# Kernel tuning notes

Measured on AMD Instinct MI355X. Metric: run time of the kernel, lower is better.

## Reference

```python
import jax, jax.numpy as jnp
import numpy as np

N = 471
TOPK = 50
T = 16384
M = 128


def setup_inputs() -> dict:
    key = jax.random.key(0)
    ks = jax.random.split(key, 6)
    x = jax.random.normal(ks[0], (T, N), dtype=jnp.float32)
    q_t = jax.random.normal(ks[1], (M, N), dtype=jnp.float32)
    # parameters, initialized as in the torch module
    w = 0.0021 + 0.0005 * jax.random.normal(ks[2], (N,), dtype=jnp.float32)
    b1 = jax.random.normal(ks[3], (N,), dtype=jnp.float32)  # unused in forward math
    alpha = jnp.array([10.0], dtype=jnp.float32)
    lamda = jnp.array([0.1], dtype=jnp.float32)
    rho = jnp.array([0.001], dtype=jnp.float32)
    mu = jnp.array([0.001], dtype=jnp.float32)
    bound = 1.0 / np.sqrt(N)
    linear_w = jax.random.uniform(ks[4], (N, N), minval=-bound, maxval=bound, dtype=jnp.float32)
    linear_b = jax.random.uniform(ks[5], (N,), minval=-bound, maxval=bound, dtype=jnp.float32)
    return {"x": x, "q_t": q_t, "w": w, "b1": b1, "alpha": alpha,
            "lamda": lamda, "rho": rho, "mu": mu,
            "linear_w": linear_w, "linear_b": linear_b}


def reference(x, q_t, w, b1, alpha, lamda, rho, mu, linear_w, linear_b):
    # W2 = mean over time of Linear(x); identical every unrolled iteration -> compute once
    W2 = (x @ linear_w.T + linear_b).mean(axis=0)           # [N]
    pinvQ = jnp.linalg.pinv(q_t @ q_t.T)                    # [M,M], identical every iter

    def theta_update(z, u):
        v = u - rho * (z - w)                               # [N]
        return alpha * (pinvQ @ (q_t @ v))                  # [M]

    def z_update(z, u, theta):
        b = w + (q_t.T @ theta) / N                         # [N]
        grad_z = W2 + rho * (z - b) + u
        grad_z = grad_z + 2.0 * lamda * (jnp.sum(z) - 1.0)  # scalar * ones broadcast
        grad_z = grad_z + 2.0 * lamda * jnp.minimum(0.0, z)
        z_new = jax.nn.relu(z - mu * grad_z)
        _, idx = jax.lax.top_k(z_new, TOPK)
        mask = jnp.zeros_like(z_new).at[idx].set(1.0)
        return z_new * mask

    z = jnp.zeros(N, dtype=x.dtype)
    u = jnp.zeros(N, dtype=x.dtype)
    for _ in range(9):
        theta = theta_update(z, u)
        z = z_update(z, u, theta)
        b = w + (q_t.T @ theta) / N
        u = u + rho * (z - b)
    theta = theta_update(z, u)
    z = z_update(z, u, theta)
    return z / (jnp.sum(z) + 1e-8)
```

## Files before the change

kernel.cpp:

```cpp
#include <hip/hip_runtime.h>

#define NDIM 471
#define MD   128
#define TD   16384
#define KSEL 50
#define CGIT 4

#define WS_PART   0
#define WS_G      120832
#define WS_T1     137216
#define WS_XBAR   197888
#define WS_W2     198400
#define WS_RW     198912
#define WS_CTR    199384
#define WS_R      199424

static __device__ __forceinline__ float rdl(float v, int lane){
    return __int_as_float(__builtin_amdgcn_readlane(__float_as_int(v), lane));
}

__global__ __launch_bounds__(512) void k_gram_colsum(const float* __restrict__ qt,
                                                     const float* __restrict__ x,
                                                     const float* __restrict__ wv,
                                                     float* __restrict__ ws){
    int lane = threadIdx.x & 63, wid = threadIdx.x >> 6;
    if (blockIdx.x < 256){
        float* G = ws + WS_G;
        int gw = blockIdx.x * 8 + wid;
        int i = gw >> 4, jb = gw & 15;
        float qi[8];
#pragma unroll
        for (int s = 0; s < 8; ++s){ int idx = lane + 64*s; qi[s] = (idx < NDIM) ? qt[i*NDIM + idx] : 0.f; }
#pragma unroll
        for (int t = 0; t < 8; ++t){
            int j = jb + 16*t;
            float acc = 0.f;
#pragma unroll
            for (int s = 0; s < 8; ++s){
                int idx = lane + 64*s;
                float qj = (idx < NDIM) ? qt[j*NDIM + idx] : 0.f;
                acc = fmaf(qi[s], qj, acc);
            }
#pragma unroll
            for (int d = 1; d < 64; d <<= 1) acc += __shfl_xor(acc, d);
            if (lane == 0) G[i*MD + j] = acc;
        }
    } else {
        int cb = blockIdx.x - 256;
        int col = threadIdx.x;
        if (col < NDIM){
            const float* xp = x + (size_t)cb*64*NDIM + col;
            float acc = 0.f;
#pragma unroll 4
            for (int r = 0; r < 64; ++r) acc += xp[(size_t)r*NDIM];
            ws[WS_PART + cb*NDIM + col] = acc;
        }
        if (cb < 16){
            int m = cb*8 + wid;
            float acc = 0.f;
#pragma unroll
            for (int s = 0; s < 8; ++s){
                int idx = lane + 64*s;
                if (idx < NDIM) acc = fmaf(qt[m*NDIM + idx], wv[idx], acc);
            }
#pragma unroll
            for (int d = 1; d < 64; d <<= 1) acc += __shfl_xor(acc, d);
            if (lane == 0) ws[WS_T1 + m] = acc;
        }
    }
}

#define G_LD(n) float4 t##n = *(const float4*)(Gp + 4*(n)); \
                float Ga##n = t##n.x, Gb##n = t##n.y, Gc##n = t##n.z, Gd##n = t##n.w;
#define G_DOT(n) pa = fmaf(Ga##n, rdl(rch.x, 2*(n)),   pa); \
                 pb = fmaf(Gb##n, rdl(rch.y, 2*(n)),   pb); \
                 pa = fmaf(Gc##n, rdl(rch.x, 2*(n)+1), pa); \
                 pb = fmaf(Gd##n, rdl(rch.y, 2*(n)+1), pb);

__global__ __launch_bounds__(256, 1) void k_cg_xbar(const float* __restrict__ qt,
                                                    const float* __restrict__ alpha,
                                                    float* __restrict__ ws){
    int tid = threadIdx.x, lane = tid & 63, wid = tid >> 6;
    if (blockIdx.x == 130 && tid == 0)
        __hip_atomic_store((unsigned*)(ws + WS_CTR), 0u, __ATOMIC_RELEASE, __HIP_MEMORY_SCOPE_AGENT);
    __shared__ __align__(16) float rl[2][2][128];
    __shared__ float part[2][2][128];
    {
        int row = tid & 127, seg = tid >> 7;
        int c   = seg;
        int col = blockIdx.x*2 + c;
        const float* Gp = ws + WS_G + row*MD + seg*64;
        G_LD(0) G_LD(1) G_LD(2)  G_LD(3)  G_LD(4)  G_LD(5)  G_LD(6)  G_LD(7)
        G_LD(8) G_LD(9) G_LD(10) G_LD(11) G_LD(12) G_LD(13) G_LD(14) G_LD(15)
        float bvv = (col < NDIM) ? qt[row*NDIM + col] : ws[WS_T1 + row];
        float xv = 0.f, rv = bvv, pv = 0.f, sv = 0.f, gam = 1.f, alf = 1.f;
        int buf = 0;
        rl[0][c][row] = rv;
        for (int it = 0; it < CGIT; ++it){
            __syncthreads();
#pragma unroll
            for (int cc = 0; cc < 2; ++cc){
                float2 rch = *(const float2*)&rl[buf][cc][seg*64 + 2*(lane & 31)];
                float pa = 0.f, pb = 0.f;
                G_DOT(0) G_DOT(1) G_DOT(2)  G_DOT(3)  G_DOT(4)  G_DOT(5)  G_DOT(6)  G_DOT(7)
                G_DOT(8) G_DOT(9) G_DOT(10) G_DOT(11) G_DOT(12) G_DOT(13) G_DOT(14) G_DOT(15)
                part[seg][cc][row] = pa + pb;
            }
            __syncthreads();
            float y = part[0][c][row] + part[1][c][row];
            float r0 = rl[buf][c][lane],      r1 = rl[buf][c][lane + 64];
            float y0 = part[0][c][lane]      + part[1][c][lane];
            float y1 = part[0][c][lane + 64] + part[1][c][lane + 64];
            float t0 = fmaf(r0, r0, r1*r1);
            float t1 = fmaf(y0, r0, y1*r1);
#pragma unroll
            for (int d = 1; d < 64; d <<= 1){ t0 += __shfl_xor(t0, d); t1 += __shfl_xor(t1, d); }
            float gp = t0, dl = t1;
            float bet, anew;
            if (it == 0){ bet = 0.f; anew = gp / fmaxf(dl, 1e-30f); }
            else { bet = gp / fmaxf(gam, 1e-30f); anew = gp / fmaxf(dl - bet*gp/alf, 1e-30f); }
            pv = fmaf(bet, pv, rv);
            sv = fmaf(bet, sv, y);
            xv = fmaf(anew, pv, xv);
            rv = fmaf(-anew, sv, rv);
            gam = gp; alf = anew;
            rl[buf^1][c][row] = rv;
            buf ^= 1;
        }
        rl[buf][c][row] = xv;
        __syncthreads();
        float sc = alpha[0] / (float)NDIM;
        float2 wc0 = ((const float2*)&rl[buf][0][0])[lane];
        float2 wc1 = ((const float2*)&rl[buf][1][0])[lane];
        int i0 = tid;
        int i1 = (tid + 256 < NDIM) ? tid + 256 : (NDIM - 1);
        float a0=0.f, a1=0.f, b0=0.f, b1=0.f;
#pragma unroll
        for (int l = 0; l < 64; ++l){
            float w0a = rdl(wc0.x, l), w0b = rdl(wc0.y, l);
            float w1a = rdl(wc1.x, l), w1b = rdl(wc1.y, l);
            float qa0 = qt[(2*l+0)*NDIM + i0], qa1 = qt[(2*l+0)*NDIM + i1];
            float qb0 = qt[(2*l+1)*NDIM + i0], qb1 = qt[(2*l+1)*NDIM + i1];
            a0 = fmaf(qa0, w0a, a0); a0 = fmaf(qb0, w0b, a0);
            a1 = fmaf(qa1, w0a, a1); a1 = fmaf(qb1, w0b, a1);
            b0 = fmaf(qa0, w1a, b0); b0 = fmaf(qb0, w1b, b0);
            b1 = fmaf(qa1, w1a, b1); b1 = fmaf(qb1, w1b, b1);
        }
        int col0 = blockIdx.x*2, col1 = col0 + 1;
        ws[WS_R + (size_t)col0*NDIM + i0] = sc*a0;
        if (tid + 256 < NDIM) ws[WS_R + (size_t)col0*NDIM + tid+256] = sc*a1;
        if (col1 < NDIM){
            ws[WS_R + (size_t)col1*NDIM + i0] = sc*b0;
            if (tid + 256 < NDIM) ws[WS_R + (size_t)col1*NDIM + tid+256] = sc*b1;
        } else {
            ws[WS_RW + i0] = sc*b0;
            if (tid + 256 < NDIM) ws[WS_RW + tid+256] = sc*b1;
        }
    }
    if (blockIdx.x < 59){
        __shared__ float p2[4][8];
        __syncthreads();
        int b2 = blockIdx.x;
        int cl = tid & 7, seg2 = tid >> 3;
        int col = b2*8 + cl;
        float acc = 0.f;
        if (col < NDIM){
#pragma unroll
            for (int q = 0; q < 8; ++q) acc += ws[WS_PART + (seg2*8 + q)*NDIM + col];
        }
        acc += __shfl_xor(acc, 8);
        acc += __shfl_xor(acc, 16);
        acc += __shfl_xor(acc, 32);
        if (lane < 8) p2[wid][lane] = acc;
        __syncthreads();
        if (tid < 8){
            float t = ((p2[0][tid] + p2[1][tid]) + (p2[2][tid] + p2[3][tid]));
            int c2 = b2*8 + tid;
            if (c2 < NDIM) ws[WS_XBAR + c2] = t * (1.0f / TD);
        }
    }
}

__global__ __launch_bounds__(512, 2) void k_w2_iter(const float* __restrict__ lw, const float* __restrict__ lb,
                                              const float* __restrict__ wv,
                                              const float* __restrict__ alpha, const float* __restrict__ lamda,
                                              const float* __restrict__ rho_p, const float* __restrict__ mu_p,
                                              float* __restrict__ ws, float* __restrict__ out){
    int tid = threadIdx.x, lane = tid & 63, wid = tid >> 6;
    unsigned* ctr = (unsigned*)(ws + WS_CTR);

    if (blockIdx.x < 59){
        int i = blockIdx.x*8 + wid;
        if (i < NDIM){
            float acc = 0.f;
#pragma unroll
            for (int s = 0; s < 8; ++s){
                int idx = lane + 64*s;
                if (idx < NDIM) acc = fmaf(lw[(size_t)i*NDIM + idx], ws[WS_XBAR + idx], acc);
            }
#pragma unroll
            for (int d = 1; d < 64; d <<= 1) acc += __shfl_xor(acc, d);
            if (lane == 0) ws[WS_W2 + i] = acc + lb[i];
        }
        __syncthreads();
        if (tid == 0)
            __hip_atomic_fetch_add(ctr, 1u, __ATOMIC_RELEASE, __HIP_MEMORY_SCOPE_AGENT);
        return;
    }

    bool act = tid < NDIM;
    int ti = act ? tid : 0;
    float rho = rho_p[0], mu = mu_p[0], lam = lamda[0];
    float sc  = alpha[0] / (float)NDIM;
    float wi  = act ? wv[tid]         : 0.f;
    float Rwi = act ? ws[WS_RW + tid] : 0.f;

    __shared__ __align__(16) unsigned bins[1024];
    __shared__ __align__(8) float2 spair[64];
    __shared__ float warr[8];
    __shared__ unsigned wcnt[8];

    bins[tid] = 0u; bins[tid + 512] = 0u;
    if (tid == 0){
        while (__hip_atomic_load(ctr, __ATOMIC_RELAXED, __HIP_MEMORY_SCOPE_AGENT) < 59u)
            __builtin_amdgcn_s_sleep(8);
        __builtin_amdgcn_fence(__ATOMIC_ACQUIRE, "agent");
    }
    __syncthreads();
    float W2i = act ? ws[WS_W2 + tid] : 0.f;

    float z = 0.f, u = 0.f, Ruv = 0.f, Rzv = 0.f, Sz = 0.f;
    unsigned tau = 0xFFFFFFFFu;
    for (int it = 0; it < 10; ++it){
        float Rv = Ruv - rho*(Rzv - Rwi);
        float b  = wi + Rv;
        float grad = W2i + rho*(z - b) + u + 2.f*lam*(Sz - 1.f);
        float zn = z - mu*grad;
        zn = (act && zn > 0.f) ? zn : 0.f;
        unsigned bits = __float_as_uint(zn);

        bool cge = act && (bits >= tau);
        unsigned long long cm = __ballot(cge);
        if (lane == 0) wcnt[wid] = (unsigned)__popcll(cm);
        __syncthreads();
        int cnt0 = 0;
#pragma unroll
        for (int w2 = 0; w2 < 8; ++w2) cnt0 += (int)wcnt[w2];
        bool fast = (cnt0 == KSEL);
        unsigned prefix = tau;

        if (!fast){
            prefix = 0; unsigned need = KSEL;
#pragma unroll
            for (int pass = 3; pass >= 0; --pass){
                int sh = pass*8;
                unsigned* bp = bins + ((3 - pass) << 8);
                bool av = (pass == 3) || ((bits >> (sh + 8)) == (prefix >> (sh + 8)));
                if (av) atomicAdd(&bp[(bits >> sh) & 255u], 1u);
                __syncthreads();
                int base = 255 - 4*lane;
                uint4 bq = *(const uint4*)&bp[base - 3];
                unsigned b3 = bq.x, b2 = bq.y, b1 = bq.z, b0 = bq.w;
                unsigned csum = b0 + b1 + b2 + b3;
                unsigned incl = csum;
#pragma unroll
                for (int d = 1; d < 64; d <<= 1){ unsigned t = __shfl_up(incl, d); if (lane >= d) incl += t; }
                unsigned excl = incl - csum;
                bool hit = (excl < need) && (need <= incl);
                unsigned long long hm = __ballot(hit);
                int hl = __ffsll((long long)hm) - 1;
                unsigned c0 = excl + b0, c1 = c0 + b1, c2 = c1 + b2;
                int byte; unsigned above, cntc;
                if      (need <= c0){ byte = base;   above = excl; cntc = b0; }
                else if (need <= c1){ byte = base-1; above = c0;   cntc = b1; }
                else if (need <= c2){ byte = base-2; above = c1;   cntc = b2; }
                else                { byte = base-3; above = c2;   cntc = b3; }
                byte  = __shfl(byte, hl);
                above = (unsigned)__shfl((int)above, hl);
                cntc  = (unsigned)__shfl((int)cntc, hl);
                prefix |= ((unsigned)byte) << sh;
                need -= above;
                if (cntc == need) break;
            }
            tau = prefix;
        }
        z = (act && bits >= prefix) ? zn : 0.f;

        bool flag = z > 0.f;
        unsigned long long mb = fast ? cm : __ballot(flag);
        float v = z;
#pragma unroll
        for (int d = 1; d < 64; d <<= 1) v += __shfl_xor(v, d);
        if (lane == 0){ warr[wid] = v; if (!fast) wcnt[wid] = (unsigned)__popcll(mb); }
        __syncthreads();
        Sz = ((warr[0]+warr[1])+(warr[2]+warr[3])) + ((warr[4]+warr[5])+(warr[6]+warr[7]));

        if (it < 9){
            unsigned off = 0;
#pragma unroll
            for (int w2 = 0; w2 < 8; ++w2) if (w2 < wid) off += wcnt[w2];
            off += (unsigned)__popcll(mb & ((1ull << lane) - 1ull));
            int cnt = 0;
#pragma unroll
            for (int w2 = 0; w2 < 8; ++w2) cnt += (int)wcnt[w2];
            if (flag){ spair[off] = make_float2(__int_as_float(tid), z); }
            if (tid >= cnt && tid < 64){ spair[tid] = make_float2(__int_as_float(0), 0.f); }
            bins[tid] = 0u; bins[tid + 512] = 0u;
            __syncthreads();

            float2 pp = spair[lane];
            const float* Rb = ws + WS_R;
            float rvv[56];
#pragma unroll
            for (int s = 0; s < 56; ++s){
                int j = __float_as_int(rdl(pp.x, s));
                rvv[s] = Rb[(size_t)j*NDIM + ti];
            }
            float a0=0.f, a1=0.f, a2=0.f, a3=0.f;
#pragma unroll
            for (int s = 0; s < 56; s += 4){
                a0 = fmaf(rvv[s+0], rdl(pp.y, s+0), a0);
                a1 = fmaf(rvv[s+1], rdl(pp.y, s+1), a1);
                a2 = fmaf(rvv[s+2], rdl(pp.y, s+2), a2);
                a3 = fmaf(rvv[s+3], rdl(pp.y, s+3), a3);
            }
            float acc = (a0+a1) + (a2+a3);
            float Rbv = Rwi + sc*Rv;
            u   += rho*(z - b);
            Ruv += rho*(acc - Rbv);
            Rzv  = acc;
        }
    }
    if (act) out[tid] = z / (Sz + 1e-8f);
}

extern "C" void kernel_launch(void* const* d_in, const int* in_sizes, int n_in,
                              void* d_out, int out_size, void* d_ws, size_t ws_size,
                              hipStream_t stream) {
    const float* x     = (const float*)d_in[0];
    const float* qt    = (const float*)d_in[1];
    const float* wv    = (const float*)d_in[2];
    const float* alpha = (const float*)d_in[4];
    const float* lamda = (const float*)d_in[5];
    const float* rho   = (const float*)d_in[6];
    const float* mu    = (const float*)d_in[7];
    const float* lw    = (const float*)d_in[8];
    const float* lb    = (const float*)d_in[9];
    float* out = (float*)d_out;
    float* ws  = (float*)d_ws;

    k_gram_colsum<<<512, 512, 0, stream>>>(qt, x, wv, ws);
    k_cg_xbar    <<<236, 256, 0, stream>>>(qt, alpha, ws);
    k_w2_iter    <<<60,  512, 0, stream>>>(lw, lb, wv, alpha, lamda, rho, mu, ws, out);
}
```

Measured before the change: 57.16 us.

## Move W2 matvec into CG kernel via grid barrier and merge top-k fast-path reductions

The W2 = linear_w·xbar matvec moves out of the iteration kernel and into the 59 xbar blocks of the CG kernel. Those blocks meet at a spin-wait atomic counter barrier before computing W2. The iteration kernel becomes a single-block launch with no spin-wait, and the counter reset moves to the first kernel. Inside the iteration loop, the fast top-k path now builds z and its sum from the threshold ballot, so one block-wide sync and reduction is skipped each iteration. The in-kernel barrier relies on all 59 blocks being co-resident, and W2 work now lengthens the CG kernel.

```diff
diff --git a/kernel.cpp b/kernel.cpp
--- a/kernel.cpp
+++ b/kernel.cpp
@@ -24,6 +24,8 @@
                                                      const float* __restrict__ wv,
                                                      float* __restrict__ ws){
     int lane = threadIdx.x & 63, wid = threadIdx.x >> 6;
+    if (blockIdx.x == 0 && threadIdx.x == 0)
+        __hip_atomic_store((unsigned*)(ws + WS_CTR), 0u, __ATOMIC_RELEASE, __HIP_MEMORY_SCOPE_AGENT);
     if (blockIdx.x < 256){
         float* G = ws + WS_G;
         int gw = blockIdx.x * 8 + wid;
@@ -79,10 +81,10 @@
 
 __global__ __launch_bounds__(256, 1) void k_cg_xbar(const float* __restrict__ qt,
                                                     const float* __restrict__ alpha,
+                                                    const float* __restrict__ lw,
+                                                    const float* __restrict__ lb,
                                                     float* __restrict__ ws){
     int tid = threadIdx.x, lane = tid & 63, wid = tid >> 6;
-    if (blockIdx.x == 130 && tid == 0)
-        __hip_atomic_store((unsigned*)(ws + WS_CTR), 0u, __ATOMIC_RELEASE, __HIP_MEMORY_SCOPE_AGENT);
     __shared__ __align__(16) float rl[2][2][128];
     __shared__ float part[2][2][128];
     {
@@ -159,6 +161,7 @@
     }
     if (blockIdx.x < 59){
         __shared__ float p2[4][8];
+        unsigned* ctr = (unsigned*)(ws + WS_CTR);
         __syncthreads();
         int b2 = blockIdx.x;
         int cl = tid & 7, seg2 = tid >> 3;
@@ -178,42 +181,43 @@
             int c2 = b2*8 + tid;
             if (c2 < NDIM) ws[WS_XBAR + c2] = t * (1.0f / TD);
         }
+        __syncthreads();
+        if (tid == 0){
+            __hip_atomic_fetch_add(ctr, 1u, __ATOMIC_RELEASE, __HIP_MEMORY_SCOPE_AGENT);
+            while (__hip_atomic_load(ctr, __ATOMIC_RELAXED, __HIP_MEMORY_SCOPE_AGENT) < 59u)
+                __builtin_amdgcn_s_sleep(2);
+            __builtin_amdgcn_fence(__ATOMIC_ACQUIRE, "agent");
+        }
+        __syncthreads();
+        for (int r = wid; r < 8; r += 4){
+            int i = b2*8 + r;
+            if (i < NDIM){
+                float acc2 = 0.f;
+#pragma unroll
+                for (int s = 0; s < 8; ++s){
+                    int idx = lane + 64*s;
+                    if (idx < NDIM) acc2 = fmaf(lw[(size_t)i*NDIM + idx], ws[WS_XBAR + idx], acc2);
+                }
+#pragma unroll
+                for (int d = 1; d < 64; d <<= 1) acc2 += __shfl_xor(acc2, d);
+                if (lane == 0) ws[WS_W2 + i] = acc2 + lb[i];
+            }
+        }
     }
 }
 
-__global__ __launch_bounds__(512, 2) void k_w2_iter(const float* __restrict__ lw, const float* __restrict__ lb,
-                                              const float* __restrict__ wv,
+__global__ __launch_bounds__(512, 2) void k_iter(const float* __restrict__ wv,
                                               const float* __restrict__ alpha, const float* __restrict__ lamda,
                                               const float* __restrict__ rho_p, const float* __restrict__ mu_p,
-                                              float* __restrict__ ws, float* __restrict__ out){
+                                              const float* __restrict__ ws, float* __restrict__ out){
     int tid = threadIdx.x, lane = tid & 63, wid = tid >> 6;
-    unsigned* ctr = (unsigned*)(ws + WS_CTR);
-
-    if (blockIdx.x < 59){
-        int i = blockIdx.x*8 + wid;
-        if (i < NDIM){
-            float acc = 0.f;
-#pragma unroll
-            for (int s = 0; s < 8; ++s){
-                int idx = lane + 64*s;
-                if (idx < NDIM) acc = fmaf(lw[(size_t)i*NDIM + idx], ws[WS_XBAR + idx], acc);
-            }
-#pragma unroll
-            for (int d = 1; d < 64; d <<= 1) acc += __shfl_xor(acc, d);
-            if (lane == 0) ws[WS_W2 + i] = acc + lb[i];
-        }
-        __syncthreads();
-        if (tid == 0)
-            __hip_atomic_fetch_add(ctr, 1u, __ATOMIC_RELEASE, __HIP_MEMORY_SCOPE_AGENT);
-        return;
-    }
-
     bool act = tid < NDIM;
     int ti = act ? tid : 0;
     float rho = rho_p[0], mu = mu_p[0], lam = lamda[0];
     float sc  = alpha[0] / (float)NDIM;
     float wi  = act ? wv[tid]         : 0.f;
     float Rwi = act ? ws[WS_RW + tid] : 0.f;
+    float W2i = act ? ws[WS_W2 + tid] : 0.f;
 
     __shared__ __align__(16) unsigned bins[1024];
     __shared__ __align__(8) float2 spair[64];
@@ -221,13 +225,7 @@
     __shared__ unsigned wcnt[8];
 
     bins[tid] = 0u; bins[tid + 512] = 0u;
-    if (tid == 0){
-        while (__hip_atomic_load(ctr, __ATOMIC_RELAXED, __HIP_MEMORY_SCOPE_AGENT) < 59u)
-            __builtin_amdgcn_s_sleep(8);
-        __builtin_amdgcn_fence(__ATOMIC_ACQUIRE, "agent");
-    }
     __syncthreads();
-    float W2i = act ? ws[WS_W2 + tid] : 0.f;
 
     float z = 0.f, u = 0.f, Ruv = 0.f, Rzv = 0.f, Sz = 0.f;
     unsigned tau = 0xFFFFFFFFu;
@@ -241,15 +239,22 @@
 
         bool cge = act && (bits >= tau);
         unsigned long long cm = __ballot(cge);
-        if (lane == 0) wcnt[wid] = (unsigned)__popcll(cm);
+        float vs = cge ? zn : 0.f;
+#pragma unroll
+        for (int d = 1; d < 64; d <<= 1) vs += __shfl_xor(vs, d);
+        if (lane == 0){ wcnt[wid] = (unsigned)__popcll(cm); warr[wid] = vs; }
         __syncthreads();
         int cnt0 = 0;
 #pragma unroll
         for (int w2 = 0; w2 < 8; ++w2) cnt0 += (int)wcnt[w2];
         bool fast = (cnt0 == KSEL);
         unsigned prefix = tau;
-
-        if (!fast){
+        unsigned long long mb;
+
+        if (fast){
+            z = cge ? zn : 0.f;
+            mb = cm;
+        } else {
             prefix = 0; unsigned need = KSEL;
 #pragma unroll
             for (int pass = 3; pass >= 0; --pass){
@@ -283,19 +288,19 @@
                 if (cntc == need) break;
             }
             tau = prefix;
-        }
-        z = (act && bits >= prefix) ? zn : 0.f;
-
-        bool flag = z > 0.f;
-        unsigned long long mb = fast ? cm : __ballot(flag);
-        float v = z;
-#pragma unroll
-        for (int d = 1; d < 64; d <<= 1) v += __shfl_xor(v, d);
-        if (lane == 0){ warr[wid] = v; if (!fast) wcnt[wid] = (unsigned)__popcll(mb); }
-        __syncthreads();
+            z = (act && bits >= prefix) ? zn : 0.f;
+            bool flag = z > 0.f;
+            mb = __ballot(flag);
+            float v = z;
+#pragma unroll
+            for (int d = 1; d < 64; d <<= 1) v += __shfl_xor(v, d);
+            if (lane == 0){ warr[wid] = v; wcnt[wid] = (unsigned)__popcll(mb); }
+            __syncthreads();
+        }
         Sz = ((warr[0]+warr[1])+(warr[2]+warr[3])) + ((warr[4]+warr[5])+(warr[6]+warr[7]));
 
         if (it < 9){
+            bool flag = z > 0.f;
             unsigned off = 0;
 #pragma unroll
             for (int w2 = 0; w2 < 8; ++w2) if (w2 < wid) off += wcnt[w2];
@@ -350,6 +355,6 @@
     float* ws  = (float*)d_ws;
 
     k_gram_colsum<<<512, 512, 0, stream>>>(qt, x, wv, ws);
-    k_cg_xbar    <<<236, 256, 0, stream>>>(qt, alpha, ws);
-    k_w2_iter    <<<60,  512, 0, stream>>>(lw, lb, wv, alpha, lamda, rho, mu, ws, out);
-}
+    k_cg_xbar    <<<236, 256, 0, stream>>>(qt, alpha, lw, lb, ws);
+    k_iter       <<<1,   512, 0, stream>>>(wv, alpha, lamda, rho, mu, ws, out);
+}
```

New measurement: 54.88 us. -4.0%, faster.
